# Optimization experiments

Measured on AMD Instinct MI355X. Metric: run time of the kernel, lower is better.

## Reference

```python
import jax, jax.numpy as jnp
import numpy as np

N = 100000   # nodes
E = 1200000  # edges
NIN, EIN = 6, 1
HID, L, H = 64, 3, 4
D = HID // H  # 16 per-head dim


def setup_inputs() -> dict:
    key = jax.random.key(0)
    ks = jax.random.split(key, 20)
    r = lambda k, shape: (jax.random.normal(k, shape, dtype=jnp.float32) * 0.1)
    inp = {
        "x": jax.random.normal(ks[0], (N, NIN), dtype=jnp.float32),
        "edge_index": jax.random.randint(ks[1], (2, E), 0, N, dtype=jnp.int64),
        "edge_attr": jax.random.normal(ks[2], (E, EIN), dtype=jnp.float32),
        # node encoder (Linear-ReLU-Linear)
        "w_ne1": r(ks[3], (NIN, HID)), "b_ne1": jnp.zeros((HID,), jnp.float32),
        "w_ne2": r(ks[4], (HID, HID)), "b_ne2": jnp.zeros((HID,), jnp.float32),
        # edge encoder (Linear)
        "w_ee": r(ks[5], (EIN, HID)), "b_ee": jnp.zeros((HID,), jnp.float32),
        # stacked GAT layers (PyG GATConv w/ edge features, concat heads)
        "w_gat": r(ks[6], (L, HID, HID)),      # node lin per layer
        "w_eg": r(ks[7], (L, HID, HID)),       # edge lin per layer
        "att_src": r(ks[8], (L, H, D)),
        "att_dst": r(ks[9], (L, H, D)),
        "att_edge": r(ks[10], (L, H, D)),
        "b_gat": jnp.zeros((L, HID), jnp.float32),
        # per-layer LayerNorm
        "ln_g": jnp.ones((L, HID), jnp.float32),
        "ln_b": jnp.zeros((L, HID), jnp.float32),
        # output projection
        "w_out": r(ks[11], (HID, HID)), "b_out": jnp.zeros((HID,), jnp.float32),
    }
    return inp


def _layernorm(x, g, b, eps=1e-5):
    m = jnp.mean(x, axis=-1, keepdims=True)
    v = jnp.mean(jnp.square(x - m), axis=-1, keepdims=True)
    return (x - m) * jax.lax.rsqrt(v + eps) * g + b


def reference(x, edge_index, edge_attr, w_ne1, b_ne1, w_ne2, b_ne2, w_ee, b_ee,
              w_gat, w_eg, att_src, att_dst, att_edge, b_gat, ln_g, ln_b,
              w_out, b_out):
    n = x.shape[0]
    src, dst = edge_index[0], edge_index[1]
    # encode nodes / edges
    h = jax.nn.relu(x @ w_ne1 + b_ne1) @ w_ne2 + b_ne2          # [N, HID]
    e = edge_attr @ w_ee + b_ee                                  # [E, HID]
    num_layers = w_gat.shape[0]
    for l in range(num_layers):
        hw = (h @ w_gat[l]).reshape(n, H, D)                     # [N,H,D]
        ew = (e @ w_eg[l]).reshape(-1, H, D)                     # [E,H,D]
        a_s = jnp.sum(hw * att_src[l], axis=-1)                  # [N,H]
        a_d = jnp.sum(hw * att_dst[l], axis=-1)                  # [N,H]
        a_e = jnp.sum(ew * att_edge[l], axis=-1)                 # [E,H]
        score = jax.nn.leaky_relu(a_s[src] + a_d[dst] + a_e, 0.2)  # [E,H]
        # softmax over incoming edges of each destination node
        smax = jax.ops.segment_max(score, dst, num_segments=n)
        ex = jnp.exp(score - smax[dst])
        den = jax.ops.segment_sum(ex, dst, num_segments=n)
        alpha = ex / (den[dst] + 1e-16)                          # [E,H]
        msg = alpha[:, :, None] * hw[src]                        # [E,H,D]
        agg = jax.ops.segment_sum(msg, dst, num_segments=n)      # [N,H,D]
        agg = agg.reshape(n, H * D) + b_gat[l]
        h = _layernorm(h + jax.nn.elu(agg), ln_g[l], ln_b[l])
    return h @ w_out + b_out
```

## Files before the change

### kernel.cpp

```cpp
#include <hip/hip_runtime.h>
#include <hip/hip_bf16.h>

#define NIN 6
#define HIDN 64
#define NHEAD 4
#define DEGPAD 5

__device__ __forceinline__ unsigned short f2bf(float f) {
    unsigned u = __float_as_uint(f);
    unsigned r = (u >> 16) & 1u;
    return (unsigned short)((u + 0x7fffu + r) >> 16);
}

__global__ __launch_bounds__(256) void encode1_kernel(
    const float* __restrict__ x,
    const float* __restrict__ w1, const float* __restrict__ b1,
    float* __restrict__ hid, int N) {
    int t = blockIdx.x * blockDim.x + threadIdx.x;
    int n = t >> 6, j = t & 63;
    if (n >= N) return;
    float acc = b1[j];
#pragma unroll
    for (int i = 0; i < NIN; i++) acc += x[n * NIN + i] * w1[i * HIDN + j];
    hid[(size_t)n * HIDN + j] = acc > 0.f ? acc : 0.f;
}

__global__ __launch_bounds__(256) void mm64_plain_kernel(
    const float* __restrict__ src, const float* __restrict__ W,
    const float* __restrict__ bias, float* __restrict__ dst, int N) {
    int j = threadIdx.x & 63;
    int wv = (blockIdx.x * blockDim.x + threadIdx.x) >> 6;
    int nw = (gridDim.x * blockDim.x) >> 6;

    float Wc[HIDN];
#pragma unroll
    for (int k = 0; k < HIDN; k++) Wc[k] = W[k * HIDN + j];
    float bj = bias[j];

    for (int n0 = wv; n0 < N; n0 += nw) {
        int n = __builtin_amdgcn_readfirstlane(n0);
        const float4* __restrict__ row = (const float4*)(src + (size_t)n * HIDN);
        float a0 = 0.f, a1 = 0.f, a2 = 0.f, a3 = 0.f;
#pragma unroll
        for (int kk = 0; kk < 16; kk++) {
            float4 r = row[kk];
            a0 += r.x * Wc[4 * kk];
            a1 += r.y * Wc[4 * kk + 1];
            a2 += r.z * Wc[4 * kk + 2];
            a3 += r.w * Wc[4 * kk + 3];
        }
        dst[(size_t)n * HIDN + j] = ((a0 + a1) + (a2 + a3)) + bj;
    }
}

__global__ __launch_bounds__(256) void mm64_attn_kernel(
    const float* __restrict__ src, const float* __restrict__ W,
    const float* __restrict__ att_s, const float* __restrict__ att_d,
    unsigned short* __restrict__ dst16,
    float* __restrict__ a_s, float* __restrict__ a_d, int N) {
    int j = threadIdx.x & 63;
    int wv = (blockIdx.x * blockDim.x + threadIdx.x) >> 6;
    int nw = (gridDim.x * blockDim.x) >> 6;

    float Wc[HIDN];
#pragma unroll
    for (int k = 0; k < HIDN; k++) Wc[k] = W[k * HIDN + j];
    float asj = att_s[j];
    float adj = att_d[j];

    for (int n0 = wv; n0 < N; n0 += nw) {
        int n = __builtin_amdgcn_readfirstlane(n0);
        const float4* __restrict__ row = (const float4*)(src + (size_t)n * HIDN);
        float a0 = 0.f, a1 = 0.f, a2 = 0.f, a3 = 0.f;
#pragma unroll
        for (int kk = 0; kk < 16; kk++) {
            float4 r = row[kk];
            a0 += r.x * Wc[4 * kk];
            a1 += r.y * Wc[4 * kk + 1];
            a2 += r.z * Wc[4 * kk + 2];
            a3 += r.w * Wc[4 * kk + 3];
        }
        float acc = (a0 + a1) + (a2 + a3);
        dst16[(size_t)n * HIDN + j] = f2bf(acc);
        float ts = acc * asj;
        float td = acc * adj;
#pragma unroll
        for (int o = 8; o > 0; o >>= 1) {
            ts += __shfl_xor(ts, o);
            td += __shfl_xor(td, o);
        }
        if ((j & 15) == 0) {
            a_s[(size_t)n * NHEAD + (j >> 4)] = ts;
            a_d[(size_t)n * NHEAD + (j >> 4)] = td;
        }
    }
}

__global__ void consts_kernel(const float* __restrict__ w_ee, const float* __restrict__ b_ee,
                              const float* __restrict__ w_eg, const float* __restrict__ att_edge,
                              float* __restrict__ c1, float* __restrict__ c0) {
    int t = threadIdx.x;
    if (t >= 12) return;
    int l = t >> 2, hh = t & 3;
    float s1 = 0.f, s0 = 0.f;
    for (int j = 0; j < HIDN; j++) {
        float wj = 0.f;
        for (int d = 0; d < 16; d++)
            wj += w_eg[l * 4096 + j * 64 + hh * 16 + d] * att_edge[l * 64 + hh * 16 + d];
        s1 += w_ee[j] * wj;
        s0 += b_ee[j] * wj;
    }
    c1[l * 4 + hh] = s1;
    c0[l * 4 + hh] = s0;
}

#define HB 8
__global__ __launch_bounds__(256) void hist_kernel(const int* __restrict__ ei,
                                                   unsigned* __restrict__ deg,
                                                   unsigned* __restrict__ rank, int E) {
    int t = blockIdx.x * 256 + threadIdx.x;
    int nt = gridDim.x * 256;
    int d[HB];
    unsigned r[HB];
#pragma unroll
    for (int k = 0; k < HB; k++) {
        int idx = t + k * nt;
        d[k] = (idx < E) ? ei[E + idx] : 0;
    }
#pragma unroll
    for (int k = 0; k < HB; k++) {
        int idx = t + k * nt;
        if (idx < E) r[k] = atomicAdd(&deg[(size_t)d[k] << DEGPAD], 1u);
    }
#pragma unroll
    for (int k = 0; k < HB; k++) {
        int idx = t + k * nt;
        if (idx < E) rank[idx] = r[k];
    }
}

__global__ __launch_bounds__(256) void scan1_kernel(const unsigned* __restrict__ deg,
                                                    unsigned* __restrict__ rp,
                                                    unsigned* __restrict__ bsum, int N) {
    __shared__ unsigned sm[256];
    int t = threadIdx.x, i = blockIdx.x * 256 + t;
    unsigned v = (i < N) ? deg[(size_t)i << DEGPAD] : 0u;
    sm[t] = v;
    __syncthreads();
    unsigned x = v;
    for (int o = 1; o < 256; o <<= 1) {
        unsigned add = (t >= o) ? sm[t - o] : 0u;
        __syncthreads();
        x += add; sm[t] = x;
        __syncthreads();
    }
    if (i < N) rp[i] = x - v;
    if (t == 255) bsum[blockIdx.x] = x;
}

__global__ void scan2_kernel(const unsigned* __restrict__ bsum,
                             unsigned* __restrict__ boff, int nb) {
    __shared__ unsigned sm[1024];
    int t = threadIdx.x;
    unsigned v = (t < nb) ? bsum[t] : 0u;
    sm[t] = v;
    __syncthreads();
    unsigned x = v;
    for (int o = 1; o < 1024; o <<= 1) {
        unsigned add = (t >= o) ? sm[t - o] : 0u;
        __syncthreads();
        x += add; sm[t] = x;
        __syncthreads();
    }
    if (t < nb) boff[t] = x - v;
}

__global__ __launch_bounds__(256) void scan3_kernel(unsigned* __restrict__ rp,
                                                    const unsigned* __restrict__ boff,
                                                    int N, int E) {
    int i = blockIdx.x * 256 + threadIdx.x;
    if (i < N) rp[i] = rp[i] + boff[blockIdx.x];
    if (i == 0) rp[N] = (unsigned)E;
}

#define SB 4
__global__ __launch_bounds__(256) void csr_scatter_kernel(
    const int* __restrict__ ei, const float* __restrict__ eattr,
    const unsigned* __restrict__ rp, const unsigned* __restrict__ rank,
    int2* __restrict__ eca, int E) {
    int t = blockIdx.x * 256 + threadIdx.x;
    int nt = gridDim.x * 256;
    int s[SB], d[SB];
    float a[SB];
    unsigned rk[SB], rpv[SB];
#pragma unroll
    for (int k = 0; k < SB; k++) {
        int idx = t + k * nt;
        if (idx < E) {
            s[k] = ei[idx];
            d[k] = ei[E + idx];
            a[k] = eattr[idx];
            rk[k] = rank[idx];
        }
    }
#pragma unroll
    for (int k = 0; k < SB; k++) {
        int idx = t + k * nt;
        if (idx < E) rpv[k] = rp[d[k]];
    }
#pragma unroll
    for (int k = 0; k < SB; k++) {
        int idx = t + k * nt;
        if (idx < E) eca[rpv[k] + rk[k]] = make_int2(s[k], __float_as_int(a[k]));
    }
}

__global__ __launch_bounds__(256) void gat_fused_kernel(
    const unsigned* __restrict__ rp, const int2* __restrict__ eca,
    const unsigned short* __restrict__ hw16,
    const float* __restrict__ a_s, const float* __restrict__ a_d,
    const float* __restrict__ c1, const float* __restrict__ c0,
    float* __restrict__ h, const float* __restrict__ bg,
    const float* __restrict__ g, const float* __restrict__ b, int N) {
    __shared__ float exl[4 * 272];
    __shared__ int srl[4 * 68];
    int t = blockIdx.x * blockDim.x + threadIdx.x;
    int lane = t & 63;
    int q = lane >> 4;
    int l = lane & 15;
    int hd = l >> 2;
    int sub = l & 3;
    int n = ((t >> 6) << 2) + q;
    int wslot = (threadIdx.x >> 6);
    float* myex = exl + wslot * 272 + 68 * q;
    int* mysrc = srl + wslot * 68 + 17 * q;

    bool nv = n < N;
    unsigned beg = nv ? rp[n] : 0u;
    int deg = nv ? (int)(rp[n + 1] - beg) : 0;

    float4 ad4 = nv ? *(const float4*)(a_d + ((size_t)n << 2)) : make_float4(0, 0, 0, 0);
    float4 C1 = *(const float4*)c1;
    float4 C0 = *(const float4*)c0;

    int md = deg;
    md = max(md, __shfl_xor(md, 16));
    md = max(md, __shfl_xor(md, 32));
    int chunks = (md + 15) >> 4;

    const unsigned* __restrict__ hwp = (const unsigned*)hw16;
    unsigned loff = (unsigned)(l << 1);

    float ssum = 0.f;
    float ac0 = 0.f, ac1 = 0.f, ac2 = 0.f, ac3 = 0.f;

    for (int k = 0; k < chunks; k++) {
        int i = (k << 4) + l;
        bool act = i < deg;
        int2 ce = act ? eca[beg + i] : make_int2(0, 0);
        int src = ce.x;
        float ea = __int_as_float(ce.y);
        float4 as4 = act ? *(const float4*)(a_s + ((size_t)src << 2))
                         : make_float4(0, 0, 0, 0);
        float s0 = as4.x + ad4.x + ea * C1.x + C0.x;
        float s1 = as4.y + ad4.y + ea * C1.y + C0.y;
        float s2 = as4.z + ad4.z + ea * C1.z + C0.z;
        float s3 = as4.w + ad4.w + ea * C1.w + C0.w;
        s0 = s0 >= 0.f ? s0 : 0.2f * s0;
        s1 = s1 >= 0.f ? s1 : 0.2f * s1;
        s2 = s2 >= 0.f ? s2 : 0.2f * s2;
        s3 = s3 >= 0.f ? s3 : 0.2f * s3;
        float e0 = act ? __expf(s0) : 0.f;
        float e1 = act ? __expf(s1) : 0.f;
        float e2 = act ? __expf(s2) : 0.f;
        float e3 = act ? __expf(s3) : 0.f;
        *(float4*)(myex + (l << 2)) = make_float4(e0, e1, e2, e3);
        mysrc[l] = act ? src : 0;

        float w0 = myex[(sub << 2) + hd];
        float w1 = myex[((sub + 4) << 2) + hd];
        float w2 = myex[((sub + 8) << 2) + hd];
        float w3 = myex[((sub + 12) << 2) + hd];
        float csum = (w0 + w1) + (w2 + w3);
        csum += __shfl_xor(csum, 1);
        csum += __shfl_xor(csum, 2);
        ssum += csum;

#pragma unroll
        for (int e = 0; e < 16; e++) {
            float w = myex[(e << 2) + hd];
            int so = mysrc[e];
            uint2 uu = *(const uint2*)(hwp + (((unsigned)so << 5) + loff));
            ac0 += w * __uint_as_float(uu.x << 16);
            ac1 += w * __uint_as_float(uu.x & 0xffff0000u);
            ac2 += w * __uint_as_float(uu.y << 16);
            ac3 += w * __uint_as_float(uu.y & 0xffff0000u);
        }
    }

    if (!nv) return;
    float inv = 1.f / (ssum + 1e-16f);
    float4 bg4 = *(const float4*)(bg + (l << 2));
    float4 hv4 = *(const float4*)(h + (size_t)n * HIDN + (l << 2));

    float a0 = ac0 * inv + bg4.x;
    float a1 = ac1 * inv + bg4.y;
    float a2 = ac2 * inv + bg4.z;
    float a3 = ac3 * inv + bg4.w;
    a0 = a0 > 0.f ? a0 : (__expf(a0) - 1.f);
    a1 = a1 > 0.f ? a1 : (__expf(a1) - 1.f);
    a2 = a2 > 0.f ? a2 : (__expf(a2) - 1.f);
    a3 = a3 > 0.f ? a3 : (__expf(a3) - 1.f);
    float v0 = hv4.x + a0, v1 = hv4.y + a1, v2 = hv4.z + a2, v3 = hv4.w + a3;

    float s = (v0 + v1) + (v2 + v3);
    float sq = (v0 * v0 + v1 * v1) + (v2 * v2 + v3 * v3);
#pragma unroll
    for (int o = 8; o > 0; o >>= 1) {
        s += __shfl_xor(s, o);
        sq += __shfl_xor(sq, o);
    }
    float mean = s * (1.f / 64.f);
    float var = sq * (1.f / 64.f) - mean * mean;
    float rr = rsqrtf(var + 1e-5f);
    float4 g4 = *(const float4*)(g + (l << 2));
    float4 b4 = *(const float4*)(b + (l << 2));
    float4 outv;
    outv.x = (v0 - mean) * rr * g4.x + b4.x;
    outv.y = (v1 - mean) * rr * g4.y + b4.y;
    outv.z = (v2 - mean) * rr * g4.z + b4.z;
    outv.w = (v3 - mean) * rr * g4.w + b4.w;
    *(float4*)(h + (size_t)n * HIDN + (l << 2)) = outv;
}

extern "C" void kernel_launch(void* const* d_in, const int* in_sizes, int n_in,
                              void* d_out, int out_size, void* d_ws, size_t ws_size,
                              hipStream_t stream) {
    const float* x      = (const float*)d_in[0];
    const int*   ei     = (const int*)d_in[1];
    const float* eattr  = (const float*)d_in[2];
    const float* w_ne1  = (const float*)d_in[3];
    const float* b_ne1  = (const float*)d_in[4];
    const float* w_ne2  = (const float*)d_in[5];
    const float* b_ne2  = (const float*)d_in[6];
    const float* w_ee   = (const float*)d_in[7];
    const float* b_ee   = (const float*)d_in[8];
    const float* w_gat  = (const float*)d_in[9];
    const float* w_eg   = (const float*)d_in[10];
    const float* att_src= (const float*)d_in[11];
    const float* att_dst= (const float*)d_in[12];
    const float* att_edge=(const float*)d_in[13];
    const float* b_gat  = (const float*)d_in[14];
    const float* ln_g   = (const float*)d_in[15];
    const float* ln_b   = (const float*)d_in[16];
    const float* w_out  = (const float*)d_in[17];
    const float* b_out  = (const float*)d_in[18];

    const int N = in_sizes[0] / NIN;
    const int E = in_sizes[2];

    float* ws   = (float*)d_ws;
    float* h    = ws;
    float* hid  = h + (size_t)N * 64;
    unsigned short* hw16 = (unsigned short*)(hid + (size_t)N * 64);
    float* a_s  = (float*)(hw16 + (size_t)N * 64);
    float* a_d  = a_s + (size_t)N * 4;
    float* c1   = a_d + (size_t)N * 4;
    float* c0   = c1 + 12;
    int2*  eca  = (int2*)(c0 + 12);
    unsigned* rank = (unsigned*)(eca + (size_t)E);
    unsigned* deg  = rank + (size_t)E;
    unsigned* rp   = deg + ((size_t)N << DEGPAD);
    unsigned* bsum = rp + (size_t)N + 1;
    unsigned* boff = bsum + 1024;

    dim3 blk(256);
    int nodeWaveBlocks = (int)(((size_t)N * 64 + 255) / 256);
    int quadBlocks = (int)(((size_t)((N + 3) / 4) * 64 + 255) / 256);
    int nodeBlocks = (N + 255) / 256;
    int histBlocks = (E + HB * 256 - 1) / (HB * 256);
    int scatBlocks = (E + SB * 256 - 1) / (SB * 256);
    int mmBlocks = 2048;

    hipMemsetAsync(deg, 0, ((size_t)N << DEGPAD) * sizeof(unsigned), stream);
    hist_kernel<<<histBlocks, blk, 0, stream>>>(ei, deg, rank, E);
    scan1_kernel<<<nodeBlocks, blk, 0, stream>>>(deg, rp, bsum, N);
    scan2_kernel<<<1, 1024, 0, stream>>>(bsum, boff, nodeBlocks);
    scan3_kernel<<<nodeBlocks, blk, 0, stream>>>(rp, boff, N, E);
    csr_scatter_kernel<<<scatBlocks, blk, 0, stream>>>(ei, eattr, rp, rank, eca, E);

    consts_kernel<<<1, 64, 0, stream>>>(w_ee, b_ee, w_eg, att_edge, c1, c0);

    encode1_kernel<<<nodeWaveBlocks, blk, 0, stream>>>(x, w_ne1, b_ne1, hid, N);
    mm64_plain_kernel<<<mmBlocks, blk, 0, stream>>>(hid, w_ne2, b_ne2, h, N);

    mm64_attn_kernel<<<mmBlocks, blk, 0, stream>>>(
        h, w_gat, att_src, att_dst, hw16, a_s, a_d, N);

    for (int l = 0; l < 3; l++) {
        gat_fused_kernel<<<quadBlocks, blk, 0, stream>>>(
            rp, eca, hw16, a_s, a_d, c1 + l * 4, c0 + l * 4,
            h, b_gat + l * 64, ln_g + l * 64, ln_b + l * 64, N);
        if (l < 2) {
            mm64_attn_kernel<<<mmBlocks, blk, 0, stream>>>(
                h, w_gat + (size_t)(l + 1) * 4096,
                att_src + (l + 1) * 64, att_dst + (l + 1) * 64,
                hw16, a_s, a_d, N);
        }
    }
    mm64_plain_kernel<<<mmBlocks, blk, 0, stream>>>(h, w_out, b_out, (float*)d_out, N);
}
```

Baseline: 501.7 us.

## Fuse histogram, node encoder, first transform and consts into one prologue kernel

Merges the degree histogram, the node encoder (both linears), the layer-0 GAT transform with attention logits, and the edge constant computation into a single block-partitioned prologue kernel. This removes the intermediate hid buffer and several launches, and lets the atomic-heavy histogram overlap with encoder compute. The per-layer matmuls now load one coalesced element per lane and broadcast it with shuffles, processing two nodes per wave iteration. The degree array loses its per-node padding, which may bring back atomic contention between neighbouring counters. HB doubles to 16 and the transform grid shrinks.

```diff
diff --git a/kernel.cpp b/kernel.cpp
--- a/kernel.cpp
+++ b/kernel.cpp
@@ -4,7 +4,8 @@
 #define NIN 6
 #define HIDN 64
 #define NHEAD 4
-#define DEGPAD 5
+#define HB 16
+#define SB 4
 
 __device__ __forceinline__ unsigned short f2bf(float f) {
     unsigned u = __float_as_uint(f);
@@ -12,93 +13,94 @@
     return (unsigned short)((u + 0x7fffu + r) >> 16);
 }
 
-__global__ __launch_bounds__(256) void encode1_kernel(
+__global__ __launch_bounds__(256, 3) void prologue_kernel(
+    const int* __restrict__ ei, unsigned* __restrict__ deg,
+    unsigned* __restrict__ rank, int E, int histB,
     const float* __restrict__ x,
     const float* __restrict__ w1, const float* __restrict__ b1,
-    float* __restrict__ hid, int N) {
-    int t = blockIdx.x * blockDim.x + threadIdx.x;
-    int n = t >> 6, j = t & 63;
-    if (n >= N) return;
-    float acc = b1[j];
-#pragma unroll
-    for (int i = 0; i < NIN; i++) acc += x[n * NIN + i] * w1[i * HIDN + j];
-    hid[(size_t)n * HIDN + j] = acc > 0.f ? acc : 0.f;
-}
-
-__global__ __launch_bounds__(256) void mm64_plain_kernel(
-    const float* __restrict__ src, const float* __restrict__ W,
-    const float* __restrict__ bias, float* __restrict__ dst, int N) {
-    int j = threadIdx.x & 63;
-    int wv = (blockIdx.x * blockDim.x + threadIdx.x) >> 6;
-    int nw = (gridDim.x * blockDim.x) >> 6;
-
-    float Wc[HIDN];
-#pragma unroll
-    for (int k = 0; k < HIDN; k++) Wc[k] = W[k * HIDN + j];
-    float bj = bias[j];
-
-    for (int n0 = wv; n0 < N; n0 += nw) {
-        int n = __builtin_amdgcn_readfirstlane(n0);
-        const float4* __restrict__ row = (const float4*)(src + (size_t)n * HIDN);
-        float a0 = 0.f, a1 = 0.f, a2 = 0.f, a3 = 0.f;
-#pragma unroll
-        for (int kk = 0; kk < 16; kk++) {
-            float4 r = row[kk];
-            a0 += r.x * Wc[4 * kk];
-            a1 += r.y * Wc[4 * kk + 1];
-            a2 += r.z * Wc[4 * kk + 2];
-            a3 += r.w * Wc[4 * kk + 3];
-        }
-        dst[(size_t)n * HIDN + j] = ((a0 + a1) + (a2 + a3)) + bj;
-    }
-}
-
-__global__ __launch_bounds__(256) void mm64_attn_kernel(
-    const float* __restrict__ src, const float* __restrict__ W,
-    const float* __restrict__ att_s, const float* __restrict__ att_d,
-    unsigned short* __restrict__ dst16,
-    float* __restrict__ a_s, float* __restrict__ a_d, int N) {
-    int j = threadIdx.x & 63;
-    int wv = (blockIdx.x * blockDim.x + threadIdx.x) >> 6;
-    int nw = (gridDim.x * blockDim.x) >> 6;
-
-    float Wc[HIDN];
-#pragma unroll
-    for (int k = 0; k < HIDN; k++) Wc[k] = W[k * HIDN + j];
-    float asj = att_s[j];
-    float adj = att_d[j];
-
-    for (int n0 = wv; n0 < N; n0 += nw) {
-        int n = __builtin_amdgcn_readfirstlane(n0);
-        const float4* __restrict__ row = (const float4*)(src + (size_t)n * HIDN);
-        float a0 = 0.f, a1 = 0.f, a2 = 0.f, a3 = 0.f;
-#pragma unroll
-        for (int kk = 0; kk < 16; kk++) {
-            float4 r = row[kk];
-            a0 += r.x * Wc[4 * kk];
-            a1 += r.y * Wc[4 * kk + 1];
-            a2 += r.z * Wc[4 * kk + 2];
-            a3 += r.w * Wc[4 * kk + 3];
-        }
-        float acc = (a0 + a1) + (a2 + a3);
-        dst16[(size_t)n * HIDN + j] = f2bf(acc);
-        float ts = acc * asj;
-        float td = acc * adj;
-#pragma unroll
-        for (int o = 8; o > 0; o >>= 1) {
-            ts += __shfl_xor(ts, o);
-            td += __shfl_xor(td, o);
-        }
-        if ((j & 15) == 0) {
-            a_s[(size_t)n * NHEAD + (j >> 4)] = ts;
-            a_d[(size_t)n * NHEAD + (j >> 4)] = td;
-        }
-    }
-}
-
-__global__ void consts_kernel(const float* __restrict__ w_ee, const float* __restrict__ b_ee,
-                              const float* __restrict__ w_eg, const float* __restrict__ att_edge,
-                              float* __restrict__ c1, float* __restrict__ c0) {
+    const float* __restrict__ w2, const float* __restrict__ b2,
+    const float* __restrict__ wg0, const float* __restrict__ atts0,
+    const float* __restrict__ attd0,
+    float* __restrict__ h, unsigned short* __restrict__ hw16,
+    float* __restrict__ a_s, float* __restrict__ a_d, int N, int encB,
+    const float* __restrict__ w_ee, const float* __restrict__ b_ee,
+    const float* __restrict__ w_eg, const float* __restrict__ att_edge,
+    float* __restrict__ c1, float* __restrict__ c0) {
+    int b = blockIdx.x;
+    if (b < histB) {
+        int t = b * 256 + threadIdx.x;
+        int nt = histB * 256;
+        int d[HB];
+        unsigned r[HB];
+#pragma unroll
+        for (int k = 0; k < HB; k++) {
+            int idx = t + k * nt;
+            d[k] = (idx < E) ? ei[E + idx] : 0;
+        }
+#pragma unroll
+        for (int k = 0; k < HB; k++) {
+            int idx = t + k * nt;
+            if (idx < E) r[k] = atomicAdd(&deg[d[k]], 1u);
+        }
+#pragma unroll
+        for (int k = 0; k < HB; k++) {
+            int idx = t + k * nt;
+            if (idx < E) rank[idx] = r[k];
+        }
+        return;
+    }
+    if (b < histB + encB) {
+        int j = threadIdx.x & 63;
+        int wv = (b - histB) * 4 + (threadIdx.x >> 6);
+        int nw = encB * 4;
+        float w1c[NIN], w2c[HIDN], wgc[HIDN];
+#pragma unroll
+        for (int i = 0; i < NIN; i++) w1c[i] = w1[i * HIDN + j];
+#pragma unroll
+        for (int k = 0; k < HIDN; k++) w2c[k] = w2[k * HIDN + j];
+#pragma unroll
+        for (int k = 0; k < HIDN; k++) wgc[k] = wg0[k * HIDN + j];
+        float b1j = b1[j], b2j = b2[j];
+        float asj = atts0[j], adj = attd0[j];
+        for (int n0 = wv; n0 < N; n0 += nw) {
+            int n = __builtin_amdgcn_readfirstlane(n0);
+            float hid = b1j;
+#pragma unroll
+            for (int i = 0; i < NIN; i++) hid += x[n * NIN + i] * w1c[i];
+            hid = hid > 0.f ? hid : 0.f;
+            float h0 = 0.f, h1 = 0.f, h2 = 0.f, h3 = 0.f;
+#pragma unroll
+            for (int k = 0; k < HIDN; k += 4) {
+                h0 += __shfl(hid, k) * w2c[k];
+                h1 += __shfl(hid, k + 1) * w2c[k + 1];
+                h2 += __shfl(hid, k + 2) * w2c[k + 2];
+                h3 += __shfl(hid, k + 3) * w2c[k + 3];
+            }
+            float hj = ((h0 + h1) + (h2 + h3)) + b2j;
+            h[(size_t)n * HIDN + j] = hj;
+            float g0 = 0.f, g1 = 0.f, g2 = 0.f, g3 = 0.f;
+#pragma unroll
+            for (int k = 0; k < HIDN; k += 4) {
+                g0 += __shfl(hj, k) * wgc[k];
+                g1 += __shfl(hj, k + 1) * wgc[k + 1];
+                g2 += __shfl(hj, k + 2) * wgc[k + 2];
+                g3 += __shfl(hj, k + 3) * wgc[k + 3];
+            }
+            float hwj = (g0 + g1) + (g2 + g3);
+            hw16[(size_t)n * HIDN + j] = f2bf(hwj);
+            float ts = hwj * asj, td = hwj * adj;
+#pragma unroll
+            for (int o = 8; o > 0; o >>= 1) {
+                ts += __shfl_xor(ts, o);
+                td += __shfl_xor(td, o);
+            }
+            if ((j & 15) == 0) {
+                a_s[(size_t)n * NHEAD + (j >> 4)] = ts;
+                a_d[(size_t)n * NHEAD + (j >> 4)] = td;
+            }
+        }
+        return;
+    }
     int t = threadIdx.x;
     if (t >= 12) return;
     int l = t >> 2, hh = t & 3;
@@ -114,28 +116,78 @@
     c0[l * 4 + hh] = s0;
 }
 
-#define HB 8
-__global__ __launch_bounds__(256) void hist_kernel(const int* __restrict__ ei,
-                                                   unsigned* __restrict__ deg,
-                                                   unsigned* __restrict__ rank, int E) {
-    int t = blockIdx.x * 256 + threadIdx.x;
-    int nt = gridDim.x * 256;
-    int d[HB];
-    unsigned r[HB];
-#pragma unroll
-    for (int k = 0; k < HB; k++) {
-        int idx = t + k * nt;
-        d[k] = (idx < E) ? ei[E + idx] : 0;
-    }
-#pragma unroll
-    for (int k = 0; k < HB; k++) {
-        int idx = t + k * nt;
-        if (idx < E) r[k] = atomicAdd(&deg[(size_t)d[k] << DEGPAD], 1u);
-    }
-#pragma unroll
-    for (int k = 0; k < HB; k++) {
-        int idx = t + k * nt;
-        if (idx < E) rank[idx] = r[k];
+__global__ __launch_bounds__(256) void xform_kernel(
+    const float* __restrict__ h, const float* __restrict__ W,
+    const float* __restrict__ att_s, const float* __restrict__ att_d,
+    unsigned short* __restrict__ dst16,
+    float* __restrict__ a_s, float* __restrict__ a_d, int N) {
+    int j = threadIdx.x & 63;
+    int wv = (blockIdx.x * blockDim.x + threadIdx.x) >> 6;
+    int nw = (gridDim.x * blockDim.x) >> 6;
+    float Wc[HIDN];
+#pragma unroll
+    for (int k = 0; k < HIDN; k++) Wc[k] = W[k * HIDN + j];
+    float asj = att_s[j], adj = att_d[j];
+    for (int n0 = wv * 2; n0 < N; n0 += nw * 2) {
+        int n1 = n0 + 1;
+        float hva = h[(size_t)n0 * HIDN + j];
+        float hvb = (n1 < N) ? h[(size_t)n1 * HIDN + j] : 0.f;
+        float a0 = 0.f, a1 = 0.f, a2 = 0.f, a3 = 0.f;
+        float c0_ = 0.f, c1_ = 0.f, c2_ = 0.f, c3_ = 0.f;
+#pragma unroll
+        for (int k = 0; k < HIDN; k += 4) {
+            a0 += __shfl(hva, k) * Wc[k];       c0_ += __shfl(hvb, k) * Wc[k];
+            a1 += __shfl(hva, k + 1) * Wc[k + 1]; c1_ += __shfl(hvb, k + 1) * Wc[k + 1];
+            a2 += __shfl(hva, k + 2) * Wc[k + 2]; c2_ += __shfl(hvb, k + 2) * Wc[k + 2];
+            a3 += __shfl(hva, k + 3) * Wc[k + 3]; c3_ += __shfl(hvb, k + 3) * Wc[k + 3];
+        }
+        float hwa = (a0 + a1) + (a2 + a3);
+        float hwb = (c0_ + c1_) + (c2_ + c3_);
+        dst16[(size_t)n0 * HIDN + j] = f2bf(hwa);
+        if (n1 < N) dst16[(size_t)n1 * HIDN + j] = f2bf(hwb);
+        float tsa = hwa * asj, tda = hwa * adj;
+        float tsb = hwb * asj, tdb = hwb * adj;
+#pragma unroll
+        for (int o = 8; o > 0; o >>= 1) {
+            tsa += __shfl_xor(tsa, o); tda += __shfl_xor(tda, o);
+            tsb += __shfl_xor(tsb, o); tdb += __shfl_xor(tdb, o);
+        }
+        if ((j & 15) == 0) {
+            a_s[(size_t)n0 * NHEAD + (j >> 4)] = tsa;
+            a_d[(size_t)n0 * NHEAD + (j >> 4)] = tda;
+            if (n1 < N) {
+                a_s[(size_t)n1 * NHEAD + (j >> 4)] = tsb;
+                a_d[(size_t)n1 * NHEAD + (j >> 4)] = tdb;
+            }
+        }
+    }
+}
+
+__global__ __launch_bounds__(256) void xform_out_kernel(
+    const float* __restrict__ h, const float* __restrict__ W,
+    const float* __restrict__ bias, float* __restrict__ out, int N) {
+    int j = threadIdx.x & 63;
+    int wv = (blockIdx.x * blockDim.x + threadIdx.x) >> 6;
+    int nw = (gridDim.x * blockDim.x) >> 6;
+    float Wc[HIDN];
+#pragma unroll
+    for (int k = 0; k < HIDN; k++) Wc[k] = W[k * HIDN + j];
+    float bj = bias[j];
+    for (int n0 = wv * 2; n0 < N; n0 += nw * 2) {
+        int n1 = n0 + 1;
+        float hva = h[(size_t)n0 * HIDN + j];
+        float hvb = (n1 < N) ? h[(size_t)n1 * HIDN + j] : 0.f;
+        float a0 = 0.f, a1 = 0.f, a2 = 0.f, a3 = 0.f;
+        float c0_ = 0.f, c1_ = 0.f, c2_ = 0.f, c3_ = 0.f;
+#pragma unroll
+        for (int k = 0; k < HIDN; k += 4) {
+            a0 += __shfl(hva, k) * Wc[k];       c0_ += __shfl(hvb, k) * Wc[k];
+            a1 += __shfl(hva, k + 1) * Wc[k + 1]; c1_ += __shfl(hvb, k + 1) * Wc[k + 1];
+            a2 += __shfl(hva, k + 2) * Wc[k + 2]; c2_ += __shfl(hvb, k + 2) * Wc[k + 2];
+            a3 += __shfl(hva, k + 3) * Wc[k + 3]; c3_ += __shfl(hvb, k + 3) * Wc[k + 3];
+        }
+        out[(size_t)n0 * HIDN + j] = (a0 + a1) + (a2 + a3) + bj;
+        if (n1 < N) out[(size_t)n1 * HIDN + j] = (c0_ + c1_) + (c2_ + c3_) + bj;
     }
 }
 
@@ -144,7 +196,7 @@
                                                     unsigned* __restrict__ bsum, int N) {
     __shared__ unsigned sm[256];
     int t = threadIdx.x, i = blockIdx.x * 256 + t;
-    unsigned v = (i < N) ? deg[(size_t)i << DEGPAD] : 0u;
+    unsigned v = (i < N) ? deg[i] : 0u;
     sm[t] = v;
     __syncthreads();
     unsigned x = v;
@@ -183,7 +235,6 @@
     if (i == 0) rp[N] = (unsigned)E;
 }
 
-#define SB 4
 __global__ __launch_bounds__(256) void csr_scatter_kernel(
     const int* __restrict__ ei, const float* __restrict__ eattr,
     const unsigned* __restrict__ rp, const unsigned* __restrict__ rank,
@@ -361,8 +412,7 @@
 
     float* ws   = (float*)d_ws;
     float* h    = ws;
-    float* hid  = h + (size_t)N * 64;
-    unsigned short* hw16 = (unsigned short*)(hid + (size_t)N * 64);
+    unsigned short* hw16 = (unsigned short*)(h + (size_t)N * 64);
     float* a_s  = (float*)(hw16 + (size_t)N * 64);
     float* a_d  = a_s + (size_t)N * 4;
     float* c1   = a_d + (size_t)N * 4;
@@ -370,43 +420,40 @@
     int2*  eca  = (int2*)(c0 + 12);
     unsigned* rank = (unsigned*)(eca + (size_t)E);
     unsigned* deg  = rank + (size_t)E;
-    unsigned* rp   = deg + ((size_t)N << DEGPAD);
+    unsigned* rp   = deg + (size_t)N;
     unsigned* bsum = rp + (size_t)N + 1;
     unsigned* boff = bsum + 1024;
 
     dim3 blk(256);
-    int nodeWaveBlocks = (int)(((size_t)N * 64 + 255) / 256);
     int quadBlocks = (int)(((size_t)((N + 3) / 4) * 64 + 255) / 256);
     int nodeBlocks = (N + 255) / 256;
-    int histBlocks = (E + HB * 256 - 1) / (HB * 256);
+    int histB = (E + HB * 256 - 1) / (HB * 256);
+    int encB = 448;
     int scatBlocks = (E + SB * 256 - 1) / (SB * 256);
-    int mmBlocks = 2048;
-
-    hipMemsetAsync(deg, 0, ((size_t)N << DEGPAD) * sizeof(unsigned), stream);
-    hist_kernel<<<histBlocks, blk, 0, stream>>>(ei, deg, rank, E);
+    int xfBlocks = 1024;
+
+    hipMemsetAsync(deg, 0, (size_t)N * sizeof(unsigned), stream);
+    prologue_kernel<<<histB + encB + 1, blk, 0, stream>>>(
+        ei, deg, rank, E, histB,
+        x, w_ne1, b_ne1, w_ne2, b_ne2, w_gat, att_src, att_dst,
+        h, hw16, a_s, a_d, N, encB,
+        w_ee, b_ee, w_eg, att_edge, c1, c0);
+
     scan1_kernel<<<nodeBlocks, blk, 0, stream>>>(deg, rp, bsum, N);
     scan2_kernel<<<1, 1024, 0, stream>>>(bsum, boff, nodeBlocks);
     scan3_kernel<<<nodeBlocks, blk, 0, stream>>>(rp, boff, N, E);
     csr_scatter_kernel<<<scatBlocks, blk, 0, stream>>>(ei, eattr, rp, rank, eca, E);
-
-    consts_kernel<<<1, 64, 0, stream>>>(w_ee, b_ee, w_eg, att_edge, c1, c0);
-
-    encode1_kernel<<<nodeWaveBlocks, blk, 0, stream>>>(x, w_ne1, b_ne1, hid, N);
-    mm64_plain_kernel<<<mmBlocks, blk, 0, stream>>>(hid, w_ne2, b_ne2, h, N);
-
-    mm64_attn_kernel<<<mmBlocks, blk, 0, stream>>>(
-        h, w_gat, att_src, att_dst, hw16, a_s, a_d, N);
 
     for (int l = 0; l < 3; l++) {
         gat_fused_kernel<<<quadBlocks, blk, 0, stream>>>(
             rp, eca, hw16, a_s, a_d, c1 + l * 4, c0 + l * 4,
             h, b_gat + l * 64, ln_g + l * 64, ln_b + l * 64, N);
         if (l < 2) {
-            mm64_attn_kernel<<<mmBlocks, blk, 0, stream>>>(
+            xform_kernel<<<xfBlocks, blk, 0, stream>>>(
                 h, w_gat + (size_t)(l + 1) * 4096,
                 att_src + (l + 1) * 64, att_dst + (l + 1) * 64,
                 hw16, a_s, a_d, N);
         }
     }
-    mm64_plain_kernel<<<mmBlocks, blk, 0, stream>>>(h, w_out, b_out, (float*)d_out, N);
-}
+    xform_out_kernel<<<xfBlocks, blk, 0, stream>>>(h, w_out, b_out, (float*)d_out, N);
+}
```

Measured after the change: 785.6 us. 1.57x slower.

## Fuse histogram, node encoder, first GAT projection and constants into one prologue kernel

Applied to the files above, without the earlier changes.

Replaces the separate histogram, consts, encode1, encoder matmul and first attention-projection kernels with a single prologue kernel. Its blocks are interleaved by role: degree-histogram blocks, fused encoder blocks that chain Linear-ReLU-Linear-GAT projection through shared memory without writing the hid buffer, and one block for the edge constants. The degree array padding is also removed, so atomics hit a dense array and the memset shrinks. This aims to cut launch overhead and intermediate memory traffic and to overlap atomic-bound and compute-bound work. The risks are more atomic contention on dense counters, and heavy register use from the two cached 64-wide weight columns in the encoder blocks.

```diff
diff --git a/kernel.cpp b/kernel.cpp
--- a/kernel.cpp
+++ b/kernel.cpp
@@ -4,7 +4,8 @@
 #define NIN 6
 #define HIDN 64
 #define NHEAD 4
-#define DEGPAD 5
+#define HB 8
+#define SB 4
 
 __device__ __forceinline__ unsigned short f2bf(float f) {
     unsigned u = __float_as_uint(f);
@@ -12,17 +13,120 @@
     return (unsigned short)((u + 0x7fffu + r) >> 16);
 }
 
-__global__ __launch_bounds__(256) void encode1_kernel(
+__global__ void prologue_kernel(
+    const int* __restrict__ ei, unsigned* __restrict__ deg,
+    unsigned* __restrict__ rank, int E, int histB,
     const float* __restrict__ x,
     const float* __restrict__ w1, const float* __restrict__ b1,
-    float* __restrict__ hid, int N) {
-    int t = blockIdx.x * blockDim.x + threadIdx.x;
-    int n = t >> 6, j = t & 63;
-    if (n >= N) return;
-    float acc = b1[j];
-#pragma unroll
-    for (int i = 0; i < NIN; i++) acc += x[n * NIN + i] * w1[i * HIDN + j];
-    hid[(size_t)n * HIDN + j] = acc > 0.f ? acc : 0.f;
+    const float* __restrict__ w2, const float* __restrict__ b2,
+    const float* __restrict__ wg0, const float* __restrict__ atts0,
+    const float* __restrict__ attd0,
+    float* __restrict__ h, unsigned short* __restrict__ hw16,
+    float* __restrict__ a_s, float* __restrict__ a_d, int N, int encB,
+    const float* __restrict__ w_ee, const float* __restrict__ b_ee,
+    const float* __restrict__ w_eg, const float* __restrict__ att_edge,
+    float* __restrict__ c1, float* __restrict__ c0) {
+    __shared__ float rowbuf[4 * HIDN];
+    int b = blockIdx.x;
+    if (b == gridDim.x - 1) {
+        int t = threadIdx.x;
+        if (t >= 12) return;
+        int l = t >> 2, hh = t & 3;
+        float s1 = 0.f, s0 = 0.f;
+        for (int j = 0; j < HIDN; j++) {
+            float wj = 0.f;
+            for (int d = 0; d < 16; d++)
+                wj += w_eg[l * 4096 + j * 64 + hh * 16 + d] * att_edge[l * 64 + hh * 16 + d];
+            s1 += w_ee[j] * wj;
+            s0 += b_ee[j] * wj;
+        }
+        c1[l * 4 + hh] = s1;
+        c0[l * 4 + hh] = s0;
+        return;
+    }
+    int grp = b / 11, r = b % 11;
+    if (r < 4) {
+        int hb = grp * 4 + r;
+        if (hb >= histB) return;
+        int t = hb * 256 + threadIdx.x;
+        int nt = histB * 256;
+        int d[HB];
+        unsigned rr[HB];
+#pragma unroll
+        for (int k = 0; k < HB; k++) {
+            int idx = t + k * nt;
+            d[k] = (idx < E) ? ei[E + idx] : 0;
+        }
+#pragma unroll
+        for (int k = 0; k < HB; k++) {
+            int idx = t + k * nt;
+            if (idx < E) rr[k] = atomicAdd(&deg[d[k]], 1u);
+        }
+#pragma unroll
+        for (int k = 0; k < HB; k++) {
+            int idx = t + k * nt;
+            if (idx < E) rank[idx] = rr[k];
+        }
+        return;
+    }
+    int eb = grp * 7 + (r - 4);
+    if (eb >= encB) return;
+    int j = threadIdx.x & 63;
+    int wslot = threadIdx.x >> 6;
+    float* row = rowbuf + wslot * HIDN;
+    int wv = eb * 4 + wslot;
+    int nw = encB * 4;
+
+    float w1c[NIN], w2c[HIDN], wgc[HIDN];
+#pragma unroll
+    for (int i = 0; i < NIN; i++) w1c[i] = w1[i * HIDN + j];
+#pragma unroll
+    for (int k = 0; k < HIDN; k++) w2c[k] = w2[k * HIDN + j];
+#pragma unroll
+    for (int k = 0; k < HIDN; k++) wgc[k] = wg0[k * HIDN + j];
+    float b1j = b1[j], b2j = b2[j];
+    float asj = atts0[j], adj = attd0[j];
+
+    for (int n = wv; n < N; n += nw) {
+        float hid = b1j;
+#pragma unroll
+        for (int i = 0; i < NIN; i++) hid += x[(size_t)n * NIN + i] * w1c[i];
+        hid = hid > 0.f ? hid : 0.f;
+        row[j] = hid;
+        float a0 = 0.f, a1 = 0.f, a2 = 0.f, a3 = 0.f;
+#pragma unroll
+        for (int kk = 0; kk < 16; kk++) {
+            float4 rv = *(const float4*)(row + kk * 4);
+            a0 += rv.x * w2c[4 * kk];
+            a1 += rv.y * w2c[4 * kk + 1];
+            a2 += rv.z * w2c[4 * kk + 2];
+            a3 += rv.w * w2c[4 * kk + 3];
+        }
+        float hj = ((a0 + a1) + (a2 + a3)) + b2j;
+        h[(size_t)n * HIDN + j] = hj;
+        row[j] = hj;
+        float g0 = 0.f, g1 = 0.f, g2 = 0.f, g3 = 0.f;
+#pragma unroll
+        for (int kk = 0; kk < 16; kk++) {
+            float4 rv = *(const float4*)(row + kk * 4);
+            g0 += rv.x * wgc[4 * kk];
+            g1 += rv.y * wgc[4 * kk + 1];
+            g2 += rv.z * wgc[4 * kk + 2];
+            g3 += rv.w * wgc[4 * kk + 3];
+        }
+        float hwj = (g0 + g1) + (g2 + g3);
+        hw16[(size_t)n * HIDN + j] = f2bf(hwj);
+        float ts = hwj * asj, td = hwj * adj;
+#pragma unroll
+        for (int o = 8; o > 0; o >>= 1) {
+            ts += __shfl_xor(ts, o);
+            td += __shfl_xor(td, o);
+        }
+        if ((j & 15) == 0) {
+            a_s[(size_t)n * NHEAD + (j >> 4)] = ts;
+            a_d[(size_t)n * NHEAD + (j >> 4)] = td;
+        }
+    }
 }
 
 __global__ __launch_bounds__(256) void mm64_plain_kernel(
@@ -96,55 +200,12 @@
     }
 }
 
-__global__ void consts_kernel(const float* __restrict__ w_ee, const float* __restrict__ b_ee,
-                              const float* __restrict__ w_eg, const float* __restrict__ att_edge,
-                              float* __restrict__ c1, float* __restrict__ c0) {
-    int t = threadIdx.x;
-    if (t >= 12) return;
-    int l = t >> 2, hh = t & 3;
-    float s1 = 0.f, s0 = 0.f;
-    for (int j = 0; j < HIDN; j++) {
-        float wj = 0.f;
-        for (int d = 0; d < 16; d++)
-            wj += w_eg[l * 4096 + j * 64 + hh * 16 + d] * att_edge[l * 64 + hh * 16 + d];
-        s1 += w_ee[j] * wj;
-        s0 += b_ee[j] * wj;
-    }
-    c1[l * 4 + hh] = s1;
-    c0[l * 4 + hh] = s0;
-}
-
-#define HB 8
-__global__ __launch_bounds__(256) void hist_kernel(const int* __restrict__ ei,
-                                                   unsigned* __restrict__ deg,
-                                                   unsigned* __restrict__ rank, int E) {
-    int t = blockIdx.x * 256 + threadIdx.x;
-    int nt = gridDim.x * 256;
-    int d[HB];
-    unsigned r[HB];
-#pragma unroll
-    for (int k = 0; k < HB; k++) {
-        int idx = t + k * nt;
-        d[k] = (idx < E) ? ei[E + idx] : 0;
-    }
-#pragma unroll
-    for (int k = 0; k < HB; k++) {
-        int idx = t + k * nt;
-        if (idx < E) r[k] = atomicAdd(&deg[(size_t)d[k] << DEGPAD], 1u);
-    }
-#pragma unroll
-    for (int k = 0; k < HB; k++) {
-        int idx = t + k * nt;
-        if (idx < E) rank[idx] = r[k];
-    }
-}
-
 __global__ __launch_bounds__(256) void scan1_kernel(const unsigned* __restrict__ deg,
                                                     unsigned* __restrict__ rp,
                                                     unsigned* __restrict__ bsum, int N) {
     __shared__ unsigned sm[256];
     int t = threadIdx.x, i = blockIdx.x * 256 + t;
-    unsigned v = (i < N) ? deg[(size_t)i << DEGPAD] : 0u;
+    unsigned v = (i < N) ? deg[i] : 0u;
     sm[t] = v;
     __syncthreads();
     unsigned x = v;
@@ -183,7 +244,6 @@
     if (i == 0) rp[N] = (unsigned)E;
 }
 
-#define SB 4
 __global__ __launch_bounds__(256) void csr_scatter_kernel(
     const int* __restrict__ ei, const float* __restrict__ eattr,
     const unsigned* __restrict__ rp, const unsigned* __restrict__ rank,
@@ -361,8 +421,7 @@
 
     float* ws   = (float*)d_ws;
     float* h    = ws;
-    float* hid  = h + (size_t)N * 64;
-    unsigned short* hw16 = (unsigned short*)(hid + (size_t)N * 64);
+    unsigned short* hw16 = (unsigned short*)(h + (size_t)N * 64);
     float* a_s  = (float*)(hw16 + (size_t)N * 64);
     float* a_d  = a_s + (size_t)N * 4;
     float* c1   = a_d + (size_t)N * 4;
@@ -370,32 +429,30 @@
     int2*  eca  = (int2*)(c0 + 12);
     unsigned* rank = (unsigned*)(eca + (size_t)E);
     unsigned* deg  = rank + (size_t)E;
-    unsigned* rp   = deg + ((size_t)N << DEGPAD);
+    unsigned* rp   = deg + (size_t)N;
     unsigned* bsum = rp + (size_t)N + 1;
     unsigned* boff = bsum + 1024;
 
     dim3 blk(256);
-    int nodeWaveBlocks = (int)(((size_t)N * 64 + 255) / 256);
     int quadBlocks = (int)(((size_t)((N + 3) / 4) * 64 + 255) / 256);
     int nodeBlocks = (N + 255) / 256;
-    int histBlocks = (E + HB * 256 - 1) / (HB * 256);
+    int histB = (E + HB * 256 - 1) / (HB * 256);
+    int grpCount = (histB + 3) / 4;
+    int encB = grpCount * 7;
     int scatBlocks = (E + SB * 256 - 1) / (SB * 256);
     int mmBlocks = 2048;
 
-    hipMemsetAsync(deg, 0, ((size_t)N << DEGPAD) * sizeof(unsigned), stream);
-    hist_kernel<<<histBlocks, blk, 0, stream>>>(ei, deg, rank, E);
+    hipMemsetAsync(deg, 0, (size_t)N * sizeof(unsigned), stream);
+    prologue_kernel<<<grpCount * 11 + 1, blk, 0, stream>>>(
+        ei, deg, rank, E, histB,
+        x, w_ne1, b_ne1, w_ne2, b_ne2, w_gat, att_src, att_dst,
+        h, hw16, a_s, a_d, N, encB,
+        w_ee, b_ee, w_eg, att_edge, c1, c0);
+
     scan1_kernel<<<nodeBlocks, blk, 0, stream>>>(deg, rp, bsum, N);
     scan2_kernel<<<1, 1024, 0, stream>>>(bsum, boff, nodeBlocks);
     scan3_kernel<<<nodeBlocks, blk, 0, stream>>>(rp, boff, N, E);
     csr_scatter_kernel<<<scatBlocks, blk, 0, stream>>>(ei, eattr, rp, rank, eca, E);
-
-    consts_kernel<<<1, 64, 0, stream>>>(w_ee, b_ee, w_eg, att_edge, c1, c0);
-
-    encode1_kernel<<<nodeWaveBlocks, blk, 0, stream>>>(x, w_ne1, b_ne1, hid, N);
-    mm64_plain_kernel<<<mmBlocks, blk, 0, stream>>>(hid, w_ne2, b_ne2, h, N);
-
-    mm64_attn_kernel<<<mmBlocks, blk, 0, stream>>>(
-        h, w_gat, att_src, att_dst, hw16, a_s, a_d, N);
 
     for (int l = 0; l < 3; l++) {
         gat_fused_kernel<<<quadBlocks, blk, 0, stream>>>(
```

After: 898.3 us. 1.79x slower.
